# Performance work log

Hardware: AMD Instinct MI355X
Metric: run time of the kernel (lower is better)

## Reference

```python
import jax, jax.numpy as jnp
import numpy as np

B, N, D, H, C, TOPK = 1, 1024, 1024, 16, 64, 2
HD = D // H   # head_dim = 64
G = N // C    # num blocks = 16


def setup_inputs() -> dict:
    key = jax.random.key(0)
    ks = jax.random.split(key, 6)
    s = 0.02  # init_std
    x = jax.random.normal(ks[0], (B, N, D), jnp.float32)
    Wq = jax.random.normal(ks[1], (D, D), jnp.float32) * s
    Wk = jax.random.normal(ks[2], (D, D), jnp.float32) * s
    Wv = jax.random.normal(ks[3], (D, D), jnp.float32) * s
    Wg = jax.random.normal(ks[4], (2 * H, D), jnp.float32) * s
    Wo = jax.random.normal(ks[5], (D, D), jnp.float32) * s
    return {"x": x, "Wq": Wq, "Wk": Wk, "Wv": Wv, "Wg": Wg, "Wo": Wo}


def reference(x, Wq, Wk, Wv, Wg, Wo):
    b, n, d = x.shape
    h, c, hd, g = H, C, HD, G
    scale = hd ** -0.5
    # projections (torch Linear: x @ W.T)
    q = (x @ Wq.T).reshape(b, n, h, hd)
    k = (x @ Wk.T).reshape(b, n, h, hd)
    v = (x @ Wv.T).reshape(b, n, h, hd)
    gate = jax.nn.softmax((x @ Wg.T).reshape(b, n, h, 2), axis=-1)
    # chunked views: (b, g, c, h, hd)
    kc = k.reshape(b, g, c, h, hd)
    vc = v.reshape(b, g, c, h, hd)
    # compressed block keys: mean over chunk dim -> (b, g, h, hd)
    k_compress = kc.mean(axis=2)
    # block selection scores (b, h, n, g)
    score = jnp.einsum('bnhd,bghd->bhng', q, k_compress)
    pos = jnp.arange(n)[:, None]
    blk = jnp.arange(g)[None, :]
    mask = pos >= c * blk  # (n, g), exactly as source's _get_mask (masked_fill where True)
    score = jnp.where(mask[None, None], -jnp.inf, score)
    idx = jax.lax.top_k(score, TOPK)[1]  # (b, h, n, top_k), int indices
    # gather selected blocks per (batch, head, query)
    k_bhgcd = kc.transpose(0, 3, 1, 2, 4)  # (b, h, g, c, hd)
    v_bhgcd = vc.transpose(0, 3, 1, 2, 4)
    gather = jax.vmap(jax.vmap(lambda kv, i: kv[i]))  # over b, h
    k_sel = gather(k_bhgcd, idx).reshape(b, h, n, TOPK * c, hd)
    v_sel = gather(v_bhgcd, idx).reshape(b, h, n, TOPK * c, hd)
    # inter: per-query attention over gathered KV (non-causal), flash-attn scale 1/sqrt(hd)
    logits = jnp.einsum('bnhd,bhnld->bhnl', q, k_sel) * scale
    p = jax.nn.softmax(logits, axis=-1)
    o_inter = jnp.einsum('bhnl,bhnld->bnhd', p, v_sel)
    # intra: causal attention within each chunk
    qc = q.reshape(b, g, c, h, hd)
    intra = jnp.einsum('bgihd,bgjhd->bghij', qc, kc) * scale
    cm = jnp.tril(jnp.ones((c, c), dtype=bool))
    intra = jnp.where(cm, intra, -jnp.inf)
    pi = jax.nn.softmax(intra, axis=-1)
    o_intra = jnp.einsum('bghij,bgjhd->bgihd', pi, vc).reshape(b, n, h, hd)
    # gated blend + output projection
    o = gate[..., 0:1] * o_inter + gate[..., 1:2] * o_intra  # (b, n, h, hd)
    return o.reshape(b, n, h * hd) @ Wo.T
```

## Files before the change

kernel.cpp:

```cpp
#include <hip/hip_runtime.h>
#include <hip/hip_bf16.h>
#include <math.h>


typedef __attribute__((ext_vector_type(8))) short short8;
typedef __attribute__((ext_vector_type(4))) float f32x4;

#define NTOK 1024
#define DMODEL 1024
#define NHEAD 16
#define HDIM 64
#define CHUNK 64
#define NBLK 16

__device__ __forceinline__ float qmax16(float v)
{
    #pragma unroll
    for (int off = 1; off < 16; off <<= 1) v = fmaxf(v, __shfl_xor(v, off));
    return v;
}

__device__ __forceinline__ float qsum16(float v)
{
    #pragma unroll
    for (int off = 1; off < 16; off <<= 1) v += __shfl_xor(v, off);
    return v;
}


#define GLOAD_LDS16(gp, lp)                                              \
    __builtin_amdgcn_global_load_lds(                                    \
        (const __attribute__((address_space(1))) void*)(gp),             \
        (__attribute__((address_space(3))) void*)(lp), 16, 0, 0)

__device__ __forceinline__ void stage64(const __hip_bfloat16* __restrict__ g0,
                                        __hip_bfloat16* t, int wave, int lane)
{
    const int sub = lane >> 3;
    const int cch = (lane & 7) ^ sub;
    #pragma unroll
    for (int j = 0; j < 2; j++) {
        const int rr = (2 * wave + j) * 8 + sub;
        GLOAD_LDS16(g0 + (size_t)rr * DMODEL + cch * 8, t + (2 * wave + j) * 512);
    }
}

__device__ __forceinline__ void stage128(const __hip_bfloat16* __restrict__ g0,
                                         __hip_bfloat16* t, int wave, int lane)
{
    const int sub = lane >> 3;
    const int cch = (lane & 7) ^ sub;
    #pragma unroll
    for (int j = 0; j < 4; j++) {
        const int grp = wave * 4 + j;
        GLOAD_LDS16(g0 + (size_t)(grp * 8 + sub) * DMODEL + cch * 8, t + grp * 512);
    }
}

__device__ __forceinline__ void stage64w8(const __hip_bfloat16* __restrict__ g0,
                                          __hip_bfloat16* t, int wave, int lane)
{
    const int sub = lane >> 3;
    const int cch = (lane & 7) ^ sub;
    GLOAD_LDS16(g0 + (size_t)(wave * 8 + sub) * DMODEL + cch * 8, t + wave * 512);
}

__device__ __forceinline__ short8 ldsfrag(const __hip_bfloat16* t, int row, int chunk)
{
    return *(const short8*)((const char*)t + row * 128 + (((chunk) ^ (row & 7)) << 4));
}

__global__ __launch_bounds__(256) void prep_kernel(
    const float* __restrict__ x,  const float* __restrict__ Wq,
    const float* __restrict__ Wk, const float* __restrict__ Wv,
    const float* __restrict__ Wo, const float* __restrict__ Wg,
    __hip_bfloat16* __restrict__ xh,  __hip_bfloat16* __restrict__ xl,
    __hip_bfloat16* __restrict__ Wqh,
    __hip_bfloat16* __restrict__ Wkh, __hip_bfloat16* __restrict__ Wvh,
    __hip_bfloat16* __restrict__ Woh, __hip_bfloat16* __restrict__ Wol,
    float* __restrict__ xm, float2* __restrict__ gate)
{
    __shared__ float gs[32];
    const int bid = blockIdx.x;
    if (bid < 5120) {
        const int which = bid >> 10;
        const int b = bid & 1023;
        const int i = (b * 256 + threadIdx.x) * 4;
        const float* in; __hip_bfloat16 *hi, *lo = nullptr;
        if (which == 0)      { in = x;  hi = xh;  lo = xl; }
        else if (which == 1) { in = Wq; hi = Wqh; }
        else if (which == 2) { in = Wk; hi = Wkh; }
        else if (which == 3) { in = Wv; hi = Wvh; }
        else                 { in = Wo; hi = Woh; lo = Wol; }
        float4 v = *(const float4*)(in + i);
        float vv[4] = {v.x, v.y, v.z, v.w};
        __hip_bfloat16 h[4], l[4];
        #pragma unroll
        for (int j = 0; j < 4; j++) {
            h[j] = __float2bfloat16(vv[j]);
            l[j] = __float2bfloat16(vv[j] - __bfloat162float(h[j]));
        }
        *(uint2*)(hi + i) = *(uint2*)h;
        if (lo) *(uint2*)(lo + i) = *(uint2*)l;
    } else if (bid < 5184) {
        const int b = bid - 5120;
        const int g = b >> 2;
        const int f = (b & 3) * 256 + threadIdx.x;
        float s = 0.f;
        #pragma unroll 8
        for (int c = 0; c < CHUNK; c++) s += x[(size_t)(g * CHUNK + c) * DMODEL + f];
        xm[g * DMODEL + f] = s * (1.0f / CHUNK);
    } else {
        const int n = bid - 5184;
        const int wave = threadIdx.x >> 6, lane = threadIdx.x & 63;
        #pragma unroll
        for (int jj = 0; jj < 8; jj++) {
            int j = wave * 8 + jj;
            float s = 0.f;
            #pragma unroll
            for (int t = 0; t < 16; t++) {
                int d = lane + (t << 6);
                s += x[n * DMODEL + d] * Wg[j * DMODEL + d];
            }
            #pragma unroll
            for (int off = 32; off; off >>= 1) s += __shfl_xor(s, off);
            if (lane == 0) gs[j] = s;
        }
        __syncthreads();
        if (threadIdx.x < NHEAD) {
            int h = threadIdx.x;
            float a = gs[2 * h], b = gs[2 * h + 1];
            float m = fmaxf(a, b);
            float ea = expf(a - m), eb = expf(b - m);
            float inv = 1.f / (ea + eb);
            gate[n * NHEAD + h] = make_float2(ea * inv, eb * inv);
        }
    }
}

__global__ __launch_bounds__(256) void kc_gemm_kernel(
    const float* __restrict__ xm, const float* __restrict__ Wk,
    float* __restrict__ kc)
{
    const int f = blockIdx.x;
    const int g = threadIdx.x >> 4;
    const int sub = threadIdx.x & 15;
    const float* wrow = Wk + (size_t)f * DMODEL;
    float s = 0.f;
    #pragma unroll 16
    for (int i = 0; i < 64; i++) {
        int e = i * 16 + sub;
        s += xm[g * DMODEL + e] * wrow[e];
    }
    #pragma unroll
    for (int off = 8; off; off >>= 1) s += __shfl_xor(s, off);
    if (sub == 0) kc[g * DMODEL + f] = s;
}

__global__ __launch_bounds__(256) void u_kernel(
    const float* __restrict__ kc, const float* __restrict__ Wq,
    __hip_bfloat16* __restrict__ Uh, __hip_bfloat16* __restrict__ Ul)
{
    __shared__ float kcs[64];
    const int h = blockIdx.x >> 4, g = blockIdx.x & 15;
    if (threadIdx.x < 64) kcs[threadIdx.x] = kc[g * DMODEL + h * HDIM + threadIdx.x];
    __syncthreads();
    const int col = (h << 4) | g;
    for (int f = threadIdx.x; f < DMODEL; f += 256) {
        float s = 0.f;
        #pragma unroll 16
        for (int d = 0; d < 64; d++)
            s += kcs[d] * Wq[(size_t)(h * HDIM + d) * DMODEL + f];
        __hip_bfloat16 hv = __float2bfloat16(s);
        Uh[(size_t)col * DMODEL + f] = hv;
        Ul[(size_t)col * DMODEL + f] = __float2bfloat16(s - __bfloat162float(hv));
    }
}

__global__ __launch_bounds__(256) void qkv_score_kernel(
    const __hip_bfloat16* __restrict__ xh, const __hip_bfloat16* __restrict__ xl,
    const __hip_bfloat16* __restrict__ Wqh, const __hip_bfloat16* __restrict__ Wkh,
    const __hip_bfloat16* __restrict__ Wvh,
    const __hip_bfloat16* __restrict__ Uh, const __hip_bfloat16* __restrict__ Ul,
    __hip_bfloat16* __restrict__ Qb, __hip_bfloat16* __restrict__ Kb,
    __hip_bfloat16* __restrict__ Vt, float* __restrict__ S)
{
    __shared__ alignas(16) char smem[65536];

    const int b = blockIdx.x;
    const int tid  = threadIdx.x;
    const int wave = tid >> 6;
    const int lane = tid & 63;
    const int fr = lane & 15;
    const int quad = lane >> 4;

    if (b < 192) {
        __hip_bfloat16* A0 = (__hip_bfloat16*)smem;
        __hip_bfloat16* B0 = (__hip_bfloat16*)(smem + 16384);
        __hip_bfloat16* A1 = (__hip_bfloat16*)(smem + 32768);
        __hip_bfloat16* B1 = (__hip_bfloat16*)(smem + 49152);

        const int widx = b >> 6;
        const int t = b & 63;
        const int m0 = (t >> 3) * 128;
        const int n0 = (t & 7) * 128;
        const __hip_bfloat16* __restrict__ Bw =
            (widx == 0) ? Wqh : (widx == 1) ? Wkh : Wvh;

        const int wm = (wave >> 1) * 64;
        const int wn = (wave & 1) * 64;

        f32x4 acc[4][4] = {};

        stage128(xh + (size_t)m0 * DMODEL, A0, wave, lane);
        stage128(Bw + (size_t)n0 * DMODEL, B0, wave, lane);
        __syncthreads();

        for (int kt = 0; kt < 16; kt++) {
            const int cur = kt & 1;
            __hip_bfloat16* Ac = cur ? A1 : A0;
            __hip_bfloat16* Bc = cur ? B1 : B0;
            if (kt < 15) {
                __hip_bfloat16* An = cur ? A0 : A1;
                __hip_bfloat16* Bn = cur ? B0 : B1;
                stage128(xh + (size_t)m0 * DMODEL + (kt + 1) * 64, An, wave, lane);
                stage128(Bw + (size_t)n0 * DMODEL + (kt + 1) * 64, Bn, wave, lane);
            }
            #pragma unroll
            for (int hk = 0; hk < 2; hk++) {
                const int ch = hk * 4 + quad;
                short8 am[4], bn[4];
                #pragma unroll
                for (int i = 0; i < 4; i++) am[i] = ldsfrag(Ac, wm + i * 16 + fr, ch);
                #pragma unroll
                for (int j = 0; j < 4; j++) bn[j] = ldsfrag(Bc, wn + j * 16 + fr, ch);
                #pragma unroll
                for (int i = 0; i < 4; i++)
                #pragma unroll
                for (int j = 0; j < 4; j++)
                    acc[i][j] = __builtin_amdgcn_mfma_f32_16x16x32_bf16(am[i], bn[j], acc[i][j], 0, 0, 0);
            }
            __syncthreads();
        }

        if (widx == 0 || widx == 1) {
            __hip_bfloat16* __restrict__ Out = (widx == 0) ? Qb : Kb;
            #pragma unroll
            for (int i = 0; i < 4; i++)
            #pragma unroll
            for (int j = 0; j < 4; j++)
            #pragma unroll
            for (int r = 0; r < 4; r++) {
                int row = m0 + wm + i * 16 + quad * 4 + r;
                int col = n0 + wn + j * 16 + fr;
                Out[(size_t)row * DMODEL + col] = __float2bfloat16(acc[i][j][r]);
            }
        } else {
            __hip_bfloat16 (*T)[136] = (__hip_bfloat16(*)[136])smem;
            for (int p = 0; p < 2; p++) {
                __syncthreads();
                if ((wn >> 6) == p) {
                    #pragma unroll
                    for (int i = 0; i < 4; i++)
                    #pragma unroll
                    for (int j = 0; j < 4; j++)
                    #pragma unroll
                    for (int r = 0; r < 4; r++) {
                        int nloc = wm + i * 16 + quad * 4 + r;
                        int floc = (wn - p * 64) + j * 16 + fr;
                        T[floc][nloc] = __float2bfloat16(acc[i][j][r]);
                    }
                }
                __syncthreads();
                const int row = tid >> 2;
                const int cb  = (tid & 3) * 32;
                const size_t o = (size_t)(n0 + p * 64 + row) * NTOK + m0 + cb;
                #pragma unroll
                for (int u = 0; u < 4; u++)
                    *(uint4*)(Vt + o + u * 8) = *(uint4*)(&T[row][cb + u * 8]);
            }
        }
    } else {
        __hip_bfloat16* AshP = (__hip_bfloat16*)smem;
        __hip_bfloat16* AslP = (__hip_bfloat16*)(smem + 8192);
        __hip_bfloat16* BshP = (__hip_bfloat16*)(smem + 16384);
        __hip_bfloat16* BslP = (__hip_bfloat16*)(smem + 24576);

        const int wm = (wave >> 1) * 32;
        const int wn = (wave & 1) * 32;

        const int bb = b - 192;
        const int m0 = (bb >> 2) * 64;
        const int n0 = (bb & 3) * 64;

        f32x4 acc[2][2] = {};

        for (int k0 = 0; k0 < DMODEL; k0 += 64) {
            stage64(xh + (size_t)m0 * DMODEL + k0, AshP, wave, lane);
            stage64(xl + (size_t)m0 * DMODEL + k0, AslP, wave, lane);
            stage64(Uh + (size_t)n0 * DMODEL + k0, BshP, wave, lane);
            stage64(Ul + (size_t)n0 * DMODEL + k0, BslP, wave, lane);
            __syncthreads();

            #pragma unroll
            for (int hk = 0; hk < 2; hk++) {
                const int ch = hk * 4 + quad;
                short8 a0h = ldsfrag(AshP, wm + fr, ch);
                short8 a1h = ldsfrag(AshP, wm + 16 + fr, ch);
                short8 a0l = ldsfrag(AslP, wm + fr, ch);
                short8 a1l = ldsfrag(AslP, wm + 16 + fr, ch);
                short8 b0h = ldsfrag(BshP, wn + fr, ch);
                short8 b1h = ldsfrag(BshP, wn + 16 + fr, ch);
                short8 b0l = ldsfrag(BslP, wn + fr, ch);
                short8 b1l = ldsfrag(BslP, wn + 16 + fr, ch);
                acc[0][0] = __builtin_amdgcn_mfma_f32_16x16x32_bf16(a0l, b0h, acc[0][0], 0, 0, 0);
                acc[0][1] = __builtin_amdgcn_mfma_f32_16x16x32_bf16(a0l, b1h, acc[0][1], 0, 0, 0);
                acc[1][0] = __builtin_amdgcn_mfma_f32_16x16x32_bf16(a1l, b0h, acc[1][0], 0, 0, 0);
                acc[1][1] = __builtin_amdgcn_mfma_f32_16x16x32_bf16(a1l, b1h, acc[1][1], 0, 0, 0);
                acc[0][0] = __builtin_amdgcn_mfma_f32_16x16x32_bf16(a0h, b0l, acc[0][0], 0, 0, 0);
                acc[0][1] = __builtin_amdgcn_mfma_f32_16x16x32_bf16(a0h, b1l, acc[0][1], 0, 0, 0);
                acc[1][0] = __builtin_amdgcn_mfma_f32_16x16x32_bf16(a1h, b0l, acc[1][0], 0, 0, 0);
                acc[1][1] = __builtin_amdgcn_mfma_f32_16x16x32_bf16(a1h, b1l, acc[1][1], 0, 0, 0);
                acc[0][0] = __builtin_amdgcn_mfma_f32_16x16x32_bf16(a0h, b0h, acc[0][0], 0, 0, 0);
                acc[0][1] = __builtin_amdgcn_mfma_f32_16x16x32_bf16(a0h, b1h, acc[0][1], 0, 0, 0);
                acc[1][0] = __builtin_amdgcn_mfma_f32_16x16x32_bf16(a1h, b0h, acc[1][0], 0, 0, 0);
                acc[1][1] = __builtin_amdgcn_mfma_f32_16x16x32_bf16(a1h, b1h, acc[1][1], 0, 0, 0);
            }
            __syncthreads();
        }

        #pragma unroll
        for (int tm = 0; tm < 2; tm++)
        #pragma unroll
        for (int tn = 0; tn < 2; tn++)
        #pragma unroll
        for (int r = 0; r < 4; r++) {
            int row = m0 + wm + tm * 16 + quad * 4 + r;
            int col = n0 + wn + tn * 16 + fr;
            S[(size_t)row * 256 + col] = acc[tm][tn][r];
        }
    }
}

__global__ __launch_bounds__(256, 4) void attn_mfma_kernel(
    const __hip_bfloat16* __restrict__ Qb, const __hip_bfloat16* __restrict__ Kb,
    const __hip_bfloat16* __restrict__ Vt, const float* __restrict__ S,
    const float2* __restrict__ gate, __hip_bfloat16* __restrict__ oh)
{
    __shared__ float OS[4][16][64];
    __shared__ float OIs[16][64];
    __shared__ float mS[4][16], lS[4][16], liS[16];
    __shared__ int i1s[16], i2s[16];
    __shared__ float2 sgate[16];
    __shared__ unsigned unionMask;
    __shared__ __hip_bfloat16 Ps[4][16][72];

    const int bid = blockIdx.x;
    const int qt = bid & 3;
    const int h  = (bid >> 2) & 15;
    const int g  = bid >> 6;
    const int tid = threadIdx.x;
    const int s = tid >> 6;
    const int lane = tid & 63;
    const int fr = lane & 15, quad = lane >> 4;

    if (tid < 16) {
        const int n = g * 64 + qt * 16 + tid;
        const float* Sn = S + (size_t)n * 256 + h * 16;
        float sc[NBLK];
        #pragma unroll
        for (int gg = 0; gg < NBLK; gg++)
            sc[gg] = (n >= (gg << 6)) ? -INFINITY : Sn[gg];
        int i1 = -1, i2 = -1;
        float b1 = -INFINITY;
        #pragma unroll
        for (int gg = 0; gg < NBLK; gg++) if (i1 < 0 || sc[gg] > b1) { b1 = sc[gg]; i1 = gg; }
        float b2 = -INFINITY;
        #pragma unroll
        for (int gg = 0; gg < NBLK; gg++) { if (gg == i1) continue; if (i2 < 0 || sc[gg] > b2) { b2 = sc[gg]; i2 = gg; } }
        i1s[tid] = i1; i2s[tid] = i2;
        sgate[tid] = gate[(size_t)n * NHEAD + h];
        unsigned m = (1u << i1) | (1u << i2);
        #pragma unroll
        for (int off = 1; off < 16; off <<= 1) m |= (unsigned)__shfl_xor((int)m, off);
        if (tid == 0) unionMask = m;
    }
    __syncthreads();

    const unsigned um = unionMask;

    const size_t qrow = (size_t)(g * 64 + qt * 16 + fr) * DMODEL + h * HDIM + quad * 8;
    const short8 qa0 = *(const short8*)(Qb + qrow);
    const short8 qa1 = *(const short8*)(Qb + qrow + 32);

    int qi1[4], qi2[4];
    #pragma unroll
    for (int r = 0; r < 4; r++) {
        int q = quad * 4 + r;
        qi1[r] = i1s[q]; qi2[r] = i2s[q];
    }

    f32x4 Oint[4] = {};
    float mrun[4] = {-INFINITY, -INFINITY, -INFINITY, -INFINITY};
    float lrun[4] = {0.f, 0.f, 0.f, 0.f};

    const __hip_bfloat16* __restrict__ Kh = Kb + h * HDIM + quad * 8;
    const __hip_bfloat16* __restrict__ Vh = Vt + (size_t)(h * HDIM) * NTOK + quad * 8;

    int j = 0;
    for (int kb = 0; kb < NBLK; kb++) {
        if (!((um >> kb) & 1u)) continue;
        if ((j++ & 3) != s) continue;

        f32x4 sacc[4] = {};
        #pragma unroll
        for (int t = 0; t < 4; t++) {
            const size_t krow = (size_t)(kb * 64 + t * 16 + fr) * DMODEL;
            short8 kb0 = *(const short8*)(Kh + krow);
            short8 kb1 = *(const short8*)(Kh + krow + 32);
            sacc[t] = __builtin_amdgcn_mfma_f32_16x16x32_bf16(qa0, kb0, sacc[t], 0, 0, 0);
            sacc[t] = __builtin_amdgcn_mfma_f32_16x16x32_bf16(qa1, kb1, sacc[t], 0, 0, 0);
        }

        #pragma unroll
        for (int r = 0; r < 4; r++) {
            const bool sel = (kb == qi1[r]) | (kb == qi2[r]);
            float v0 = sacc[0][r] * 0.125f, v1 = sacc[1][r] * 0.125f;
            float v2 = sacc[2][r] * 0.125f, v3 = sacc[3][r] * 0.125f;
            float mx = qmax16(fmaxf(fmaxf(v0, v1), fmaxf(v2, v3)));
            float mnew = sel ? fmaxf(mrun[r], mx) : mrun[r];
            float f = sel ? __expf(mrun[r] - mnew) : 1.0f;
            float e0 = sel ? __expf(v0 - mnew) : 0.f;
            float e1 = sel ? __expf(v1 - mnew) : 0.f;
            float e2 = sel ? __expf(v2 - mnew) : 0.f;
            float e3 = sel ? __expf(v3 - mnew) : 0.f;
            float es = qsum16(e0 + e1 + e2 + e3);
            lrun[r] = lrun[r] * f + es;
            mrun[r] = mnew;
            #pragma unroll
            for (int dn = 0; dn < 4; dn++) Oint[dn][r] *= f;
            const int prow = quad * 4 + r;
            Ps[s][prow][ 0 + fr] = __float2bfloat16(e0);
            Ps[s][prow][16 + fr] = __float2bfloat16(e1);
            Ps[s][prow][32 + fr] = __float2bfloat16(e2);
            Ps[s][prow][48 + fr] = __float2bfloat16(e3);
        }

        short8 pa0 = *(const short8*)(&Ps[s][fr][quad * 8]);
        short8 pa1 = *(const short8*)(&Ps[s][fr][32 + quad * 8]);
        #pragma unroll
        for (int dn = 0; dn < 4; dn++) {
            const size_t vrow = (size_t)(dn * 16 + fr) * NTOK + kb * 64;
            short8 v0 = *(const short8*)(Vh + vrow);
            short8 v1 = *(const short8*)(Vh + vrow + 32);
            Oint[dn] = __builtin_amdgcn_mfma_f32_16x16x32_bf16(pa0, v0, Oint[dn], 0, 0, 0);
            Oint[dn] = __builtin_amdgcn_mfma_f32_16x16x32_bf16(pa1, v1, Oint[dn], 0, 0, 0);
        }
    }

    if ((j & 3) == s) {
        f32x4 sacc[4] = {};
        #pragma unroll
        for (int t = 0; t < 4; t++) {
            const size_t krow = (size_t)(g * 64 + t * 16 + fr) * DMODEL;
            short8 kb0 = *(const short8*)(Kh + krow);
            short8 kb1 = *(const short8*)(Kh + krow + 32);
            sacc[t] = __builtin_amdgcn_mfma_f32_16x16x32_bf16(qa0, kb0, sacc[t], 0, 0, 0);
            sacc[t] = __builtin_amdgcn_mfma_f32_16x16x32_bf16(qa1, kb1, sacc[t], 0, 0, 0);
        }
        f32x4 Ointr[4] = {};
        #pragma unroll
        for (int r = 0; r < 4; r++) {
            const int qloc = qt * 16 + quad * 4 + r;
            float vv[4];
            #pragma unroll
            for (int t = 0; t < 4; t++) {
                const int col = t * 16 + fr;
                float v = sacc[t][r] * 0.125f;
                vv[t] = (col <= qloc) ? v : -INFINITY;
            }
            float mx = qmax16(fmaxf(fmaxf(vv[0], vv[1]), fmaxf(vv[2], vv[3])));
            float e0 = __expf(vv[0] - mx), e1 = __expf(vv[1] - mx);
            float e2 = __expf(vv[2] - mx), e3 = __expf(vv[3] - mx);
            float lsum = qsum16(e0 + e1 + e2 + e3);
            const int prow = quad * 4 + r;
            if (fr == 0) liS[prow] = lsum;
            Ps[s][prow][ 0 + fr] = __float2bfloat16(e0);
            Ps[s][prow][16 + fr] = __float2bfloat16(e1);
            Ps[s][prow][32 + fr] = __float2bfloat16(e2);
            Ps[s][prow][48 + fr] = __float2bfloat16(e3);
        }
        short8 pa0 = *(const short8*)(&Ps[s][fr][quad * 8]);
        short8 pa1 = *(const short8*)(&Ps[s][fr][32 + quad * 8]);
        f32x4 Ointr2[4] = {};
        #pragma unroll
        for (int dn = 0; dn < 4; dn++) {
            const size_t vrow = (size_t)(dn * 16 + fr) * NTOK + g * 64;
            short8 v0 = *(const short8*)(Vh + vrow);
            short8 v1 = *(const short8*)(Vh + vrow + 32);
            Ointr2[dn] = __builtin_amdgcn_mfma_f32_16x16x32_bf16(pa0, v0, Ointr[dn], 0, 0, 0);
            Ointr2[dn] = __builtin_amdgcn_mfma_f32_16x16x32_bf16(pa1, v1, Ointr2[dn], 0, 0, 0);
        }
        #pragma unroll
        for (int r = 0; r < 4; r++)
        #pragma unroll
        for (int dn = 0; dn < 4; dn++)
            OIs[quad * 4 + r][dn * 16 + fr] = Ointr2[dn][r];
    }

    #pragma unroll
    for (int r = 0; r < 4; r++) {
        if (fr == 0) { mS[s][quad * 4 + r] = mrun[r]; lS[s][quad * 4 + r] = lrun[r]; }
        #pragma unroll
        for (int dn = 0; dn < 4; dn++)
            OS[s][quad * 4 + r][dn * 16 + fr] = Oint[dn][r];
    }
    __syncthreads();

    {
        const int q = tid >> 4;
        const int db = (tid & 15) * 4;
        float M = fmaxf(fmaxf(mS[0][q], mS[1][q]), fmaxf(mS[2][q], mS[3][q]));
        float L = 0.f;
        float o0 = 0.f, o1 = 0.f, o2 = 0.f, o3 = 0.f;
        #pragma unroll
        for (int ss = 0; ss < 4; ss++) {
            float p = __expf(mS[ss][q] - M);
            L += lS[ss][q] * p;
            o0 += OS[ss][q][db + 0] * p;
            o1 += OS[ss][q][db + 1] * p;
            o2 += OS[ss][q][db + 2] * p;
            o3 += OS[ss][q][db + 3] * p;
        }
        const float2 gt = sgate[q];
        const float wi = gt.x / L;
        const float wl = gt.y / liS[q];
        unsigned short out4[4];
        out4[0] = __builtin_bit_cast(unsigned short, __float2bfloat16(wi * o0 + wl * OIs[q][db + 0]));
        out4[1] = __builtin_bit_cast(unsigned short, __float2bfloat16(wi * o1 + wl * OIs[q][db + 1]));
        out4[2] = __builtin_bit_cast(unsigned short, __float2bfloat16(wi * o2 + wl * OIs[q][db + 2]));
        out4[3] = __builtin_bit_cast(unsigned short, __float2bfloat16(wi * o3 + wl * OIs[q][db + 3]));
        const int n = g * 64 + qt * 16 + q;
        *(uint2*)(oh + (size_t)n * DMODEL + h * HDIM + db) = *(uint2*)out4;
    }
}

__global__ __launch_bounds__(512) void gemm_wo(
    const __hip_bfloat16* __restrict__ Ah,
    const __hip_bfloat16* __restrict__ Bh, const __hip_bfloat16* __restrict__ Bl,
    float* __restrict__ C)
{
    __shared__ alignas(16) char smem[24576];
    __hip_bfloat16* AshP = (__hip_bfloat16*)smem;
    __hip_bfloat16* BshP = (__hip_bfloat16*)(smem + 8192);
    __hip_bfloat16* BslP = (__hip_bfloat16*)(smem + 16384);

    const int n0 = blockIdx.x * 64;
    const int m0 = blockIdx.y * 64;

    const int tid  = threadIdx.x;
    const int wave = tid >> 6;
    const int lane = tid & 63;
    const int wm = (wave >> 1) * 16;
    const int wn = (wave & 1) * 32;
    const int fr = lane & 15;
    const int quad = lane >> 4;

    f32x4 acc[2] = {};

    for (int k0 = 0; k0 < DMODEL; k0 += 64) {
        stage64w8(Ah + (size_t)m0 * DMODEL + k0, AshP, wave, lane);
        stage64w8(Bh + (size_t)n0 * DMODEL + k0, BshP, wave, lane);
        stage64w8(Bl + (size_t)n0 * DMODEL + k0, BslP, wave, lane);
        __syncthreads();

        #pragma unroll
        for (int hk = 0; hk < 2; hk++) {
            const int ch = hk * 4 + quad;
            short8 a0  = ldsfrag(AshP, wm + fr, ch);
            short8 b0h = ldsfrag(BshP, wn + fr, ch);
            short8 b1h = ldsfrag(BshP, wn + 16 + fr, ch);
            short8 b0l = ldsfrag(BslP, wn + fr, ch);
            short8 b1l = ldsfrag(BslP, wn + 16 + fr, ch);
            acc[0] = __builtin_amdgcn_mfma_f32_16x16x32_bf16(a0, b0l, acc[0], 0, 0, 0);
            acc[1] = __builtin_amdgcn_mfma_f32_16x16x32_bf16(a0, b1l, acc[1], 0, 0, 0);
            acc[0] = __builtin_amdgcn_mfma_f32_16x16x32_bf16(a0, b0h, acc[0], 0, 0, 0);
            acc[1] = __builtin_amdgcn_mfma_f32_16x16x32_bf16(a0, b1h, acc[1], 0, 0, 0);
        }
        __syncthreads();
    }

    #pragma unroll
    for (int tn = 0; tn < 2; tn++)
    #pragma unroll
    for (int r = 0; r < 4; r++) {
        int row = m0 + wm + quad * 4 + r;
        int col = n0 + wn + tn * 16 + fr;
        C[(size_t)row * DMODEL + col] = acc[tn][r];
    }
}

extern "C" void kernel_launch(void* const* d_in, const int* in_sizes, int n_in,
                              void* d_out, int out_size, void* d_ws, size_t ws_size,
                              hipStream_t stream)
{
    const float* x  = (const float*)d_in[0];
    const float* Wq = (const float*)d_in[1];
    const float* Wk = (const float*)d_in[2];
    const float* Wv = (const float*)d_in[3];
    const float* Wg = (const float*)d_in[4];
    const float* Wo = (const float*)d_in[5];

    const size_t M1 = (size_t)NTOK * DMODEL;

    float* S       = (float*)d_ws;
    float* xm      = S + (size_t)NTOK * 256;
    float* kc      = xm + NBLK * DMODEL;
    float2* gate   = (float2*)(kc + NBLK * DMODEL);
    __hip_bfloat16* xh  = (__hip_bfloat16*)(gate + NTOK * NHEAD);
    __hip_bfloat16* xl  = xh + M1;
    __hip_bfloat16* Wqh = xl + M1;
    __hip_bfloat16* Wkh = Wqh + M1;
    __hip_bfloat16* Wvh = Wkh + M1;
    __hip_bfloat16* Woh = Wvh + M1;
    __hip_bfloat16* Wol = Woh + M1;
    __hip_bfloat16* oh  = Wol + M1;
    __hip_bfloat16* Uh  = oh + M1;
    __hip_bfloat16* Ul  = Uh + 256 * DMODEL;
    __hip_bfloat16* Qb  = Ul + 256 * DMODEL;
    __hip_bfloat16* Kb  = Qb + M1;
    __hip_bfloat16* Vt  = Kb + M1;

    prep_kernel<<<6208, 256, 0, stream>>>(
        x, Wq, Wk, Wv, Wo, Wg, xh, xl, Wqh, Wkh, Wvh, Woh, Wol, xm, gate);

    kc_gemm_kernel<<<1024, 256, 0, stream>>>(xm, Wk, kc);
    u_kernel<<<256, 256, 0, stream>>>(kc, Wq, Uh, Ul);

    qkv_score_kernel<<<256, 256, 0, stream>>>(
        xh, xl, Wqh, Wkh, Wvh, Uh, Ul, Qb, Kb, Vt, S);

    attn_mfma_kernel<<<NBLK * NHEAD * 4, 256, 0, stream>>>(Qb, Kb, Vt, S, gate, oh);

    dim3 gwo(16, 16);
    gemm_wo<<<gwo, 512, 0, stream>>>(oh, Woh, Wol, (float*)d_out);
}
```

Baseline: 158.9 us.

## Use fine-grained vmcnt waits and double-buffer the Wo GEMM staging

The QKV projection GEMM replaces __syncthreads with explicit s_waitcnt vmcnt counts plus raw s_barrier, so the prefetch of the next K tile can stay in flight while the current tile is computed. The Wo GEMM gains a second LDS buffer set and the same prefetch pattern, overlapping global loads with MFMA work. The trade-off is double the LDS in gemm_wo, which may lower occupancy. Correctness depends on the hard-coded vmcnt values matching how many loads stage128 and stage64w8 actually issue, and on those helpers loading straight to LDS.

Result: faster. 155.2 us (-2.4%).

```diff
diff --git a/kernel.cpp b/kernel.cpp
--- a/kernel.cpp
+++ b/kernel.cpp
@@ -214,7 +214,9 @@
 
         stage128(xh + (size_t)m0 * DMODEL, A0, wave, lane);
         stage128(Bw + (size_t)n0 * DMODEL, B0, wave, lane);
-        __syncthreads();
+        asm volatile("s_waitcnt vmcnt(0)" ::: "memory");
+        __builtin_amdgcn_sched_barrier(0);
+        __builtin_amdgcn_s_barrier();
 
         for (int kt = 0; kt < 16; kt++) {
             const int cur = kt & 1;
@@ -225,7 +227,14 @@
                 __hip_bfloat16* Bn = cur ? B0 : B1;
                 stage128(xh + (size_t)m0 * DMODEL + (kt + 1) * 64, An, wave, lane);
                 stage128(Bw + (size_t)n0 * DMODEL + (kt + 1) * 64, Bn, wave, lane);
+                asm volatile("s_waitcnt vmcnt(8)" ::: "memory");
+            } else {
+                asm volatile("s_waitcnt vmcnt(0)" ::: "memory");
             }
+            __builtin_amdgcn_sched_barrier(0);
+            __builtin_amdgcn_s_barrier();
+            __builtin_amdgcn_sched_barrier(0);
+
             #pragma unroll
             for (int hk = 0; hk < 2; hk++) {
                 const int ch = hk * 4 + quad;
@@ -240,7 +249,9 @@
                 for (int j = 0; j < 4; j++)
                     acc[i][j] = __builtin_amdgcn_mfma_f32_16x16x32_bf16(am[i], bn[j], acc[i][j], 0, 0, 0);
             }
-            __syncthreads();
+            __builtin_amdgcn_sched_barrier(0);
+            __builtin_amdgcn_s_barrier();
+            __builtin_amdgcn_sched_barrier(0);
         }
 
         if (widx == 0 || widx == 1) {
@@ -550,10 +561,13 @@
     const __hip_bfloat16* __restrict__ Bh, const __hip_bfloat16* __restrict__ Bl,
     float* __restrict__ C)
 {
-    __shared__ alignas(16) char smem[24576];
-    __hip_bfloat16* AshP = (__hip_bfloat16*)smem;
-    __hip_bfloat16* BshP = (__hip_bfloat16*)(smem + 8192);
-    __hip_bfloat16* BslP = (__hip_bfloat16*)(smem + 16384);
+    __shared__ alignas(16) char smem[49152];
+    __hip_bfloat16* As0 = (__hip_bfloat16*)smem;
+    __hip_bfloat16* Bh0 = (__hip_bfloat16*)(smem + 8192);
+    __hip_bfloat16* Bl0 = (__hip_bfloat16*)(smem + 16384);
+    __hip_bfloat16* As1 = (__hip_bfloat16*)(smem + 24576);
+    __hip_bfloat16* Bh1 = (__hip_bfloat16*)(smem + 32768);
+    __hip_bfloat16* Bl1 = (__hip_bfloat16*)(smem + 40960);
 
     const int n0 = blockIdx.x * 64;
     const int m0 = blockIdx.y * 64;
@@ -568,26 +582,49 @@
 
     f32x4 acc[2] = {};
 
-    for (int k0 = 0; k0 < DMODEL; k0 += 64) {
-        stage64w8(Ah + (size_t)m0 * DMODEL + k0, AshP, wave, lane);
-        stage64w8(Bh + (size_t)n0 * DMODEL + k0, BshP, wave, lane);
-        stage64w8(Bl + (size_t)n0 * DMODEL + k0, BslP, wave, lane);
-        __syncthreads();
+    stage64w8(Ah + (size_t)m0 * DMODEL, As0, wave, lane);
+    stage64w8(Bh + (size_t)n0 * DMODEL, Bh0, wave, lane);
+    stage64w8(Bl + (size_t)n0 * DMODEL, Bl0, wave, lane);
+    asm volatile("s_waitcnt vmcnt(0)" ::: "memory");
+    __builtin_amdgcn_sched_barrier(0);
+    __builtin_amdgcn_s_barrier();
+
+    for (int kt = 0; kt < 16; kt++) {
+        const int cur = kt & 1;
+        __hip_bfloat16* Ac  = cur ? As1 : As0;
+        __hip_bfloat16* Bhc = cur ? Bh1 : Bh0;
+        __hip_bfloat16* Blc = cur ? Bl1 : Bl0;
+        if (kt < 15) {
+            __hip_bfloat16* An  = cur ? As0 : As1;
+            __hip_bfloat16* Bhn = cur ? Bh0 : Bh1;
+            __hip_bfloat16* Bln = cur ? Bl0 : Bl1;
+            stage64w8(Ah + (size_t)m0 * DMODEL + (kt + 1) * 64, An, wave, lane);
+            stage64w8(Bh + (size_t)n0 * DMODEL + (kt + 1) * 64, Bhn, wave, lane);
+            stage64w8(Bl + (size_t)n0 * DMODEL + (kt + 1) * 64, Bln, wave, lane);
+            asm volatile("s_waitcnt vmcnt(3)" ::: "memory");
+        } else {
+            asm volatile("s_waitcnt vmcnt(0)" ::: "memory");
+        }
+        __builtin_amdgcn_sched_barrier(0);
+        __builtin_amdgcn_s_barrier();
+        __builtin_amdgcn_sched_barrier(0);
 
         #pragma unroll
         for (int hk = 0; hk < 2; hk++) {
             const int ch = hk * 4 + quad;
-            short8 a0  = ldsfrag(AshP, wm + fr, ch);
-            short8 b0h = ldsfrag(BshP, wn + fr, ch);
-            short8 b1h = ldsfrag(BshP, wn + 16 + fr, ch);
-            short8 b0l = ldsfrag(BslP, wn + fr, ch);
-            short8 b1l = ldsfrag(BslP, wn + 16 + fr, ch);
+            short8 a0  = ldsfrag(Ac, wm + fr, ch);
+            short8 b0h = ldsfrag(Bhc, wn + fr, ch);
+            short8 b1h = ldsfrag(Bhc, wn + 16 + fr, ch);
+            short8 b0l = ldsfrag(Blc, wn + fr, ch);
+            short8 b1l = ldsfrag(Blc, wn + 16 + fr, ch);
             acc[0] = __builtin_amdgcn_mfma_f32_16x16x32_bf16(a0, b0l, acc[0], 0, 0, 0);
             acc[1] = __builtin_amdgcn_mfma_f32_16x16x32_bf16(a0, b1l, acc[1], 0, 0, 0);
             acc[0] = __builtin_amdgcn_mfma_f32_16x16x32_bf16(a0, b0h, acc[0], 0, 0, 0);
             acc[1] = __builtin_amdgcn_mfma_f32_16x16x32_bf16(a0, b1h, acc[1], 0, 0, 0);
         }
-        __syncthreads();
+        __builtin_amdgcn_sched_barrier(0);
+        __builtin_amdgcn_s_barrier();
+        __builtin_amdgcn_sched_barrier(0);
     }
 
     #pragma unroll
```
